# Optimization experiments

Hardware: AMD Instinct MI355X
Metric: run time of the kernel (lower is better)

## Reference

```python
import jax, jax.numpy as jnp
import numpy as np

IMG = 640
C = 256
A = 9
NC = 80
K = 1000          # max candidates kept into NMS (fixed for jit)
SCORE_TH = 0.05
IOU_TH = 0.5
STRIDES = (8, 16, 32, 64, 128)
SIZES = (32, 64, 128, 256, 512)


def conv3(x, w, b):
    # x: [N,C,H,W], w: [O,I,3,3]
    y = jax.lax.conv_general_dilated(x, w, (1, 1), 'SAME',
                                     dimension_numbers=('NCHW', 'OIHW', 'NCHW'))
    return y + b[None, :, None, None]


def head(x, ws, bs, hw, hb):
    for i in range(4):
        x = jax.nn.relu(conv3(x, ws[i], bs[i]))
    return conv3(x, hw, hb)


def classifier(x, ws, bs, hw, hb):
    y = jax.nn.sigmoid(head(x, ws, bs, hw, hb))          # [N, A*NC, H, W]
    n, _, h, w = y.shape
    y = y.transpose(0, 2, 3, 1).reshape(n, h, w, A, NC)  # NHWA,NC ordering as in torch view
    return y.reshape(n, -1, NC)


def regressor(x, ws, bs, hw, hb):
    y = head(x, ws, bs, hw, hb)                           # [N, A*4, H, W]
    n, _, h, w = y.shape
    return y.transpose(0, 2, 3, 1).reshape(n, -1, 4)


def make_anchors():
    ratios = jnp.array([0.5, 1.0, 2.0], jnp.float32)
    scales = jnp.array([1.0, 2.0 ** (1.0 / 3.0), 2.0 ** (2.0 / 3.0)], jnp.float32)
    levels = []
    for stride, size in zip(STRIDES, SIZES):
        ws = (size * scales[None, :]) / jnp.sqrt(ratios[:, None])  # [3,3]
        hs = (size * scales[None, :]) * jnp.sqrt(ratios[:, None])
        ws, hs = ws.reshape(-1), hs.reshape(-1)                    # [9]
        fs = IMG // stride
        c = (jnp.arange(fs, dtype=jnp.float32) + 0.5) * stride
        cy, cx = jnp.meshgrid(c, c, indexing='ij')                 # [H,W]
        cx, cy = cx[..., None], cy[..., None]                      # [H,W,1]
        boxes = jnp.stack([cx - ws / 2, cy - hs / 2, cx + ws / 2, cy + hs / 2], -1)  # [H,W,9,4]
        levels.append(boxes.reshape(-1, 4))
    return jnp.concatenate(levels, 0)  # [76725, 4]


def decode_clip(anchors, loc):
    # BBoxTransform with std (0.1,0.1,0.2,0.2), then ClipBoxes to image
    w = anchors[:, 2] - anchors[:, 0]
    h = anchors[:, 3] - anchors[:, 1]
    cx = anchors[:, 0] + 0.5 * w
    cy = anchors[:, 1] + 0.5 * h
    dx, dy = loc[:, 0] * 0.1, loc[:, 1] * 0.1
    dw, dh = loc[:, 2] * 0.2, loc[:, 3] * 0.2
    pcx, pcy = cx + dx * w, cy + dy * h
    pw, ph = jnp.exp(dw) * w, jnp.exp(dh) * h
    boxes = jnp.stack([pcx - 0.5 * pw, pcy - 0.5 * ph, pcx + 0.5 * pw, pcy + 0.5 * ph], -1)
    return jnp.clip(boxes, 0.0, float(IMG))


def nms_keep(boxes, valid):
    # boxes [K,4] sorted by descending score, valid [K] bool; greedy NMS keep mask
    x1, y1, x2, y2 = boxes[:, 0], boxes[:, 1], boxes[:, 2], boxes[:, 3]
    area = jnp.maximum(x2 - x1, 0.0) * jnp.maximum(y2 - y1, 0.0)
    xx1 = jnp.maximum(x1[:, None], x1[None, :])
    yy1 = jnp.maximum(y1[:, None], y1[None, :])
    xx2 = jnp.minimum(x2[:, None], x2[None, :])
    yy2 = jnp.minimum(y2[:, None], y2[None, :])
    inter = jnp.maximum(xx2 - xx1, 0.0) * jnp.maximum(yy2 - yy1, 0.0)
    iou = inter / (area[:, None] + area[None, :] - inter + 1e-8)
    idx = jnp.arange(boxes.shape[0])

    def body(i, keep):
        sup = (iou[i] > IOU_TH) & (idx > i) & keep[i]
        return keep & ~sup

    return jax.lax.fori_loop(0, boxes.shape[0], body, valid)


def forward(p3, p4, p5, p6, p7, cls_w, cls_b, cls_hw, cls_hb, reg_w, reg_b, reg_hw, reg_hb):
    feats = [p3, p4, p5, p6, p7]
    cls_pred = jnp.concatenate([classifier(f, cls_w, cls_b, cls_hw, cls_hb) for f in feats], 1)[0]  # [N_anch, NC]
    loc_pred = jnp.concatenate([regressor(f, reg_w, reg_b, reg_hw, reg_hb) for f in feats], 1)[0]   # [N_anch, 4]
    anchors = make_anchors()
    boxes = decode_clip(anchors, loc_pred)
    scores = jnp.max(cls_pred, axis=1)                     # [N_anch]
    masked = jnp.where(scores > SCORE_TH, scores, -1.0)
    top_vals, top_idx = jax.lax.top_k(masked, K)
    valid = top_vals > 0.0
    sel_boxes = boxes[top_idx]                             # [K,4]
    keep = nms_keep(sel_boxes, valid)
    sel_cls = cls_pred[top_idx]                            # [K,NC]
    nms_scores = jnp.where(keep, top_vals, 0.0)
    nms_classes = jnp.argmax(sel_cls, axis=1).astype(jnp.int32)
    nms_boxes = jnp.where(keep[:, None], sel_boxes, 0.0)
    return nms_scores, nms_classes, nms_boxes, keep


def setup_inputs() -> dict:
    key = jax.random.key(0)
    ks = jax.random.split(key, 12)
    inp = {}
    for i, (name, hw_) in enumerate(zip(['p3', 'p4', 'p5', 'p6', 'p7'], [80, 40, 20, 10, 5])):
        inp[name] = jax.random.normal(ks[i], (1, C, hw_, hw_), jnp.float32)
    inp['cls_w'] = jax.random.normal(ks[5], (4, C, C, 3, 3), jnp.float32) * 0.05
    inp['cls_b'] = jnp.zeros((4, C), jnp.float32)
    inp['cls_hw'] = jax.random.normal(ks[6], (A * NC, C, 3, 3), jnp.float32) * 0.05
    inp['cls_hb'] = jnp.full((A * NC,), -2.0, jnp.float32)
    inp['reg_w'] = jax.random.normal(ks[7], (4, C, C, 3, 3), jnp.float32) * 0.05
    inp['reg_b'] = jnp.zeros((4, C), jnp.float32)
    inp['reg_hw'] = jax.random.normal(ks[8], (36, C, 3, 3), jnp.float32) * 0.05
    inp['reg_hb'] = jnp.zeros((36,), jnp.float32)
    return inp


def reference(p3, p4, p5, p6, p7, cls_w, cls_b, cls_hw, cls_hb, reg_w, reg_b, reg_hw, reg_hb):
    return forward(p3, p4, p5, p6, p7, cls_w, cls_b, cls_hw, cls_hb, reg_w, reg_b, reg_hw, reg_hb)
```

## Files before the change

### kernel.cpp

```cpp
#include <hip/hip_runtime.h>
#include <math.h>
#include <stdint.h>

#define NANCH 76725
#define NPAD  131072
#define NPAD2 32768
#define PXTOT 8525

typedef _Float16 half8 __attribute__((ext_vector_type(8)));
typedef _Float16 half4 __attribute__((ext_vector_type(4)));
typedef float float4v __attribute__((ext_vector_type(4)));
typedef unsigned long long u64;

#define ACT2_EL  ((size_t)PXTOT * 512)
#define HEADC_EL (720 * PXTOT)
#define HEADR_EL (36 * PXTOT)

#define TRUNK_WP_EL (9 * 2 * 8 * 16 * 64 * 8)
#define CLSH_WP_EL  (9 * 2 * 8 * 48 * 64 * 8)
#define REGH_WP_EL  (9 * 2 * 8 * 4 * 64 * 8)

struct PrepArgs {
    const float* src[10];
    _Float16*    dst[10];
    int Co[10], NC16[10];
    long base[11];
};

__global__ __launch_bounds__(256) void prep_k(PrepArgs P)
{
    long idx = (long)blockIdx.x * 256 + threadIdx.x;
    if (idx >= P.base[10]) return;
    int e = 0;
    while (idx >= P.base[e + 1]) e++;
    long local = idx - P.base[e];
    const int NC16 = P.NC16[e], Co = P.Co[e];
    int lane = (int)(local & 63);
    long t2 = local >> 6;
    int c16 = (int)(t2 % NC16);
    long t3 = t2 / NC16;
    int cc = (int)(t3 & 7);
    int t4 = (int)(t3 >> 3);
    int s = t4 & 1, tap = t4 >> 1;
    int co = c16 * 16 + (lane & 15);
    int kb = cc * 32 + (lane >> 4) * 8;
    const float* src = P.src[e];
    half8 out;
#pragma unroll
    for (int j = 0; j < 8; j++) {
        float v = (co < Co) ? src[(size_t)(co * 256 + kb + j) * 9 + tap] : 0.f;
        _Float16 h = (_Float16)v;
        out[j] = s ? (_Float16)(v - (float)h) : h;
    }
    _Float16* dst = P.dst[e] + ((((size_t)(tap * 2 + s) * 8 + cc) * NC16 + c16) * 64 + lane) * 8;
    *(half8*)dst = out;
}

struct RepArgs { const float* src[5]; _Float16* dst; };

__global__ __launch_bounds__(256) void repack_k(RepArgs R)
{
    __shared__ float T[64][257];
    const int cumT[5] = {100, 125, 132, 134, 135};
    const int Wt[5]   = {80, 40, 20, 10, 5};
    const int pxB[5]  = {0, 6400, 8000, 8400, 8500};
    int t = blockIdx.x;
    int lv = 0; while (t >= cumT[lv]) lv++;
    int tile = t - (lv ? cumT[lv - 1] : 0);
    const int HW = Wt[lv] * Wt[lv];
    const int pxStart = tile * 64;
    const float* src = R.src[lv];
    const int tid = threadIdx.x, w = tid >> 6, l6 = tid & 63;
    int p = pxStart + l6;
    bool ok = p < HW;
    for (int ci = w; ci < 256; ci += 4)
        T[l6][ci] = ok ? src[(size_t)ci * HW + p] : 0.f;
    __syncthreads();
    _Float16* dst = R.dst + (size_t)pxB[lv] * 512;
    for (int px = w; px < 64; px += 4) {
        int pp = pxStart + px;
        if (pp >= HW) continue;
        half4 h, l;
#pragma unroll
        for (int j = 0; j < 4; j++) {
            float v = T[px][l6 * 4 + j];
            _Float16 hh = (_Float16)v;
            h[j] = hh; l[j] = (_Float16)(v - (float)hh);
        }
        *(half4*)(dst + (size_t)pp * 512 + l6 * 4) = h;
        *(half4*)(dst + (size_t)pp * 512 + 256 + l6 * 4) = l;
    }
}

struct C3Args {
    const _Float16* aIn0; const _Float16* aIn1;
    _Float16* aOut0; _Float16* aOut1;
    float* hOut0; float* hOut1;
    const _Float16* wp0; const _Float16* wp1;
    const float* bias0; const float* bias1;
    int CoPad0, CoPad1, Co0, Co1, mode;
};

__global__ __launch_bounds__(256, 4) void conv3_k(C3Args A)
{
    const int cumT[5] = {200, 250, 265, 271, 273};
    const int txA[5]  = {10, 5, 3, 2, 1};
    const int Wt[5]   = {80, 40, 20, 10, 5};
    const int pxB[5]  = {0, 6400, 8000, 8400, 8500};

    __shared__ __align__(16) _Float16 Xs[60 * 72];

    const int gid = blockIdx.x;
    int head, coGrp, t;
    if (A.mode == 0) {
        int oct = gid & 7; head = oct >> 2; int tq = oct & 3;
        int p = gid >> 3; coGrp = p & 1; int tl = p >> 1;
        t = tq * 69 + tl;
    } else {
        int oct = gid & 7; int tq = oct & 3; int ch = oct >> 2;
        int p = gid >> 3; int ci = p & 3; int tl = p >> 2;
        int combo = ch * 4 + ci;
        if (combo >= 7) return;
        head = (combo == 6) ? 1 : 0;
        coGrp = (combo == 6) ? 0 : combo;
        t = tq * 69 + tl;
    }
    if (t >= 273) return;

    int lv = 0; while (t >= cumT[lv]) lv++;
    const int tile = t - (lv ? cumT[lv - 1] : 0);
    const int W = Wt[lv], HW = W * W;
    const int tx = txA[lv];
    const int tyi = tile / tx, txi = tile - tyi * tx;
    const int x0 = txi * 8, y0 = tyi * 4;

    const _Float16* aIn = (head ? A.aIn1 : A.aIn0) + (size_t)pxB[lv] * 512;
    const _Float16* wp  = head ? A.wp1 : A.wp0;
    const float* bias   = head ? A.bias1 : A.bias0;
    const int CoPad     = head ? A.CoPad1 : A.CoPad0;
    const int Co        = head ? A.Co1 : A.Co0;
    const int NC16      = CoPad >> 4;

    const int tid = threadIdx.x;
    const int w = tid >> 6, lane = tid & 63;
    const int l15 = lane & 15, quad = lane >> 4;
    const int coW = coGrp * 128 + w * 32;
    const bool active = coW < CoPad;
    const int c16b = coW >> 4;

    float4v acc[2][2];
#pragma unroll
    for (int i = 0; i < 2; i++)
#pragma unroll
        for (int j = 0; j < 2; j++) acc[i][j] = (float4v){0.f, 0.f, 0.f, 0.f};

    const half8 z8 = {(_Float16)0, (_Float16)0, (_Float16)0, (_Float16)0,
                      (_Float16)0, (_Float16)0, (_Float16)0, (_Float16)0};

    for (int cc = 0; cc < 8; cc++) {
        const int ci0 = cc * 32;
        __syncthreads();
        {
            int u0 = tid, u1 = tid + 256;
            int px0 = u0 >> 3, sg0 = u0 & 7;
            int r0 = px0 / 10, c0 = px0 - r0 * 10;
            int gy0 = y0 + r0 - 1, gx0 = x0 + c0 - 1;
            bool v0ok = (gy0 >= 0) && (gy0 < W) && (gx0 >= 0) && (gx0 < W);
            int e0 = (sg0 < 4) ? (ci0 + sg0 * 8) : (256 + ci0 + (sg0 - 4) * 8);
            int gp0 = v0ok ? (gy0 * W + gx0) : 0;
            half8 v0 = v0ok ? *(const half8*)(aIn + (size_t)gp0 * 512 + e0) : z8;

            bool u1v = u1 < 480;
            int px1 = u1 >> 3, sg1 = u1 & 7;
            int r1 = px1 / 10, c1 = px1 - r1 * 10;
            int gy1 = y0 + r1 - 1, gx1 = x0 + c1 - 1;
            bool v1ok = u1v && (gy1 >= 0) && (gy1 < W) && (gx1 >= 0) && (gx1 < W);
            int e1 = (sg1 < 4) ? (ci0 + sg1 * 8) : (256 + ci0 + (sg1 - 4) * 8);
            int gp1 = v1ok ? (gy1 * W + gx1) : 0;
            half8 v1 = v1ok ? *(const half8*)(aIn + (size_t)gp1 * 512 + e1) : z8;

            *(half8*)(Xs + px0 * 72 + sg0 * 8) = v0;
            if (u1v) *(half8*)(Xs + px1 * 72 + sg1 * 8) = v1;
        }
        __syncthreads();

        if (active) {
            for (int tap = 0; tap < 9; tap++) {
                const int dy = tap / 3 - 1, dx = tap % 3 - 1;
                half8 ah[2], al[2];
#pragma unroll
                for (int mf = 0; mf < 2; mf++) {
                    int lpx = (2 * mf + (l15 >> 3) + 1 + dy) * 10 + (l15 & 7) + 1 + dx;
                    const _Float16* lp = Xs + lpx * 72 + quad * 8;
                    ah[mf] = *(const half8*)lp;
                    al[mf] = *(const half8*)(lp + 32);
                }
                half8 bh[2], bl[2];
#pragma unroll
                for (int nf = 0; nf < 2; nf++) {
                    const _Float16* wb = wp +
                        ((((size_t)(tap * 2) * 8 + cc) * NC16 + c16b + nf) * 64 + lane) * 8;
                    bh[nf] = *(const half8*)wb;
                    bl[nf] = *(const half8*)(wb + (size_t)4096 * NC16);
                }
#pragma unroll
                for (int nf = 0; nf < 2; nf++) {
#pragma unroll
                    for (int mf = 0; mf < 2; mf++) {
                        acc[mf][nf] = __builtin_amdgcn_mfma_f32_16x16x32_f16(ah[mf], bh[nf], acc[mf][nf], 0, 0, 0);
                        acc[mf][nf] = __builtin_amdgcn_mfma_f32_16x16x32_f16(ah[mf], bl[nf], acc[mf][nf], 0, 0, 0);
                        acc[mf][nf] = __builtin_amdgcn_mfma_f32_16x16x32_f16(al[mf], bh[nf], acc[mf][nf], 0, 0, 0);
                    }
                }
            }
        }
    }

    if (!active) return;

    int coN[2];
    float bv[2];
#pragma unroll
    for (int nf = 0; nf < 2; nf++) {
        coN[nf] = coW + nf * 16 + l15;
        bv[nf] = (coN[nf] < Co) ? bias[coN[nf]] : 0.f;
    }

    if (A.mode == 0) {
        _Float16* ao = (head ? A.aOut1 : A.aOut0) + (size_t)pxB[lv] * 512;
#pragma unroll
        for (int nf = 0; nf < 2; nf++) {
#pragma unroll
            for (int mf = 0; mf < 2; mf++) {
#pragma unroll
                for (int r = 0; r < 4; r++) {
                    int m = quad * 4 + r;
                    int yy = y0 + 2 * mf + (m >> 3);
                    int xx = x0 + (m & 7);
                    if (yy < W && xx < W) {
                        int px = yy * W + xx;
                        float v = fmaxf(acc[mf][nf][r] + bv[nf], 0.f);
                        _Float16 h = (_Float16)v;
                        _Float16 lo = (_Float16)(v - (float)h);
                        ao[(size_t)px * 512 + coN[nf]] = h;
                        ao[(size_t)px * 512 + 256 + coN[nf]] = lo;
                    }
                }
            }
        }
    } else {
        float* ho = (head ? A.hOut1 : A.hOut0) + (size_t)Co * pxB[lv];
#pragma unroll
        for (int nf = 0; nf < 2; nf++) {
            if (coN[nf] < Co) {
                float* col = ho + (size_t)coN[nf] * HW;
#pragma unroll
                for (int mf = 0; mf < 2; mf++) {
#pragma unroll
                    for (int r = 0; r < 4; r++) {
                        int m = quad * 4 + r;
                        int yy = y0 + 2 * mf + (m >> 3);
                        int xx = x0 + (m & 7);
                        if (yy < W && xx < W) col[yy * W + xx] = acc[mf][nf][r] + bv[nf];
                    }
                }
            }
        }
    }
}

__global__ void cls_reduce_k(const float* __restrict__ ho,
                             u64* __restrict__ keys, int* __restrict__ cls_all)
{
    const int cumB[5] = {225, 282, 297, 301, 302};
    const int HWs[5]  = {6400, 1600, 400, 100, 25};
    const int pxB[5]  = {0, 6400, 8000, 8400, 8500};
    const int offs[5] = {0, 57600, 72000, 75600, 76500};
    int b = blockIdx.x;
    int lv = 0;
    while (b >= cumB[lv]) lv++;
    int local = (b - (lv ? cumB[lv - 1] : 0)) * 256 + threadIdx.x;
    const int HW = HWs[lv];
    if (local >= HW * 9) return;
    int a = local / HW, p = local - a * HW;
    const float* base = ho + (size_t)720 * pxB[lv] + (size_t)a * 80 * HW + p;
    float m = -1.f; int arg = 0;
    for (int c = 0; c < 80; c++) {
        float logit = base[(size_t)c * HW];
        float s = 1.0f / (1.0f + expf(-logit));
        if (s > m) { m = s; arg = c; }
    }
    float masked = (m > 0.05f) ? m : -1.0f;
    unsigned u = __float_as_uint(masked);
    unsigned su = (u & 0x80000000u) ? ~u : (u | 0x80000000u);
    int g = offs[lv] + p * 9 + a;
    keys[g] = ((u64)su << 32) | (u64)(0xFFFFFFFFu - (unsigned)g);
    cls_all[g] = arg;
}

struct DecArgs { float aw[45]; float ah[45]; };

__global__ void decode_k(const float* __restrict__ ro, DecArgs D, float* __restrict__ boxes_all)
{
    const int cumB[5] = {225, 282, 297, 301, 302};
    const int HWs[5]  = {6400, 1600, 400, 100, 25};
    const int Wt[5]   = {80, 40, 20, 10, 5};
    const int pxB[5]  = {0, 6400, 8000, 8400, 8500};
    const int offs[5] = {0, 57600, 72000, 75600, 76500};
    const float strd[5] = {8.f, 16.f, 32.f, 64.f, 128.f};
    int b = blockIdx.x;
    int lv = 0;
    while (b >= cumB[lv]) lv++;
    int local = (b - (lv ? cumB[lv - 1] : 0)) * 256 + threadIdx.x;
    const int HW = HWs[lv], W = Wt[lv];
    if (local >= HW * 9) return;
    int a = local / HW, p = local - a * HW;
    int y = p / W, x = p - y * W;
    float cx0 = ((float)x + 0.5f) * strd[lv];
    float cy0 = ((float)y + 0.5f) * strd[lv];
    float aw = D.aw[lv * 9 + a], ahh = D.ah[lv * 9 + a];
    float ax1 = cx0 - aw * 0.5f, ax2 = cx0 + aw * 0.5f;
    float ay1 = cy0 - ahh * 0.5f, ay2 = cy0 + ahh * 0.5f;
    float w = ax2 - ax1, h = ay2 - ay1;
    float cx = ax1 + 0.5f * w, cy = ay1 + 0.5f * h;
    const float* base = ro + (size_t)36 * pxB[lv] + p;
    float l0 = base[(size_t)(a * 4 + 0) * HW];
    float l1 = base[(size_t)(a * 4 + 1) * HW];
    float l2 = base[(size_t)(a * 4 + 2) * HW];
    float l3 = base[(size_t)(a * 4 + 3) * HW];
    float dx = l0 * 0.1f, dy = l1 * 0.1f, dw = l2 * 0.2f, dh = l3 * 0.2f;
    float pcx = cx + dx * w, pcy = cy + dy * h;
    float pw = expf(dw) * w, ph = expf(dh) * h;
    float bx1 = fminf(fmaxf(pcx - 0.5f * pw, 0.f), 640.f);
    float by1 = fminf(fmaxf(pcy - 0.5f * ph, 0.f), 640.f);
    float bx2 = fminf(fmaxf(pcx + 0.5f * pw, 0.f), 640.f);
    float by2 = fminf(fmaxf(pcy + 0.5f * ph, 0.f), 640.f);
    int g = offs[lv] + p * 9 + a;
    boxes_all[g * 4 + 0] = bx1;
    boxes_all[g * 4 + 1] = by1;
    boxes_all[g * 4 + 2] = bx2;
    boxes_all[g * 4 + 3] = by2;
}

__global__ void pad_keys_k(u64* __restrict__ keys)
{
    int i = blockIdx.x * blockDim.x + threadIdx.x + NANCH;
    if (i < NPAD) keys[i] = 0ULL;
}

__global__ __launch_bounds__(1024) void chunk_sort_desc_k(u64* __restrict__ keys)
{
    __shared__ u64 s[4096];
    const int base = blockIdx.x * 4096;
    for (int i = threadIdx.x; i < 4096; i += 1024) s[i] = keys[base + i];
    __syncthreads();
    for (int size = 2; size <= 4096; size <<= 1) {
        for (int stride = size >> 1; stride > 0; stride >>= 1) {
            for (int t = threadIdx.x; t < 2048; t += 1024) {
                int low = t & (stride - 1);
                int i = ((t - low) << 1) | low;
                int j = i + stride;
                bool desc = ((i & size) == 0);
                u64 a = s[i], b = s[j];
                if (desc ? (a < b) : (a > b)) { s[i] = b; s[j] = a; }
            }
            __syncthreads();
        }
    }
    for (int i = threadIdx.x; i < 4096; i += 1024) keys[base + i] = s[i];
}

__global__ __launch_bounds__(1024) void gather_top_k(const u64* __restrict__ keys,
                                                     u64* __restrict__ keys2)
{
    int i = blockIdx.x * 1024 + threadIdx.x;
    keys2[i] = keys[(i >> 10) * 4096 + (i & 1023)];
}

__global__ void bitonic_global_k(u64* __restrict__ keys, int size, int stride)
{
    int t = blockIdx.x * blockDim.x + threadIdx.x;
    int low = t & (stride - 1);
    int i = ((t - low) << 1) | low;
    int j = i + stride;
    bool desc = ((i & size) == 0);
    u64 a = keys[i], b = keys[j];
    if (desc ? (a < b) : (a > b)) { keys[i] = b; keys[j] = a; }
}

__global__ __launch_bounds__(1024) void bitonic_local_full_k(u64* __restrict__ keys)
{
    __shared__ u64 s[4096];
    const int base = blockIdx.x * 4096;
    for (int i = threadIdx.x; i < 4096; i += 1024) s[i] = keys[base + i];
    __syncthreads();
    for (int size = 2; size <= 4096; size <<= 1) {
        for (int stride = size >> 1; stride > 0; stride >>= 1) {
            for (int t = threadIdx.x; t < 2048; t += 1024) {
                int low = t & (stride - 1);
                int i = ((t - low) << 1) | low;
                int j = i + stride;
                bool desc = (((base + i) & size) == 0);
                u64 a = s[i], b = s[j];
                if (desc ? (a < b) : (a > b)) { s[i] = b; s[j] = a; }
            }
            __syncthreads();
        }
    }
    for (int i = threadIdx.x; i < 4096; i += 1024) keys[base + i] = s[i];
}

__global__ __launch_bounds__(1024) void bitonic_local_k(u64* __restrict__ keys, int size)
{
    __shared__ u64 s[4096];
    const int base = blockIdx.x * 4096;
    for (int i = threadIdx.x; i < 4096; i += 1024) s[i] = keys[base + i];
    __syncthreads();
    const bool desc = ((base & size) == 0);
    for (int stride = 2048; stride > 0; stride >>= 1) {
        for (int t = threadIdx.x; t < 2048; t += 1024) {
            int low = t & (stride - 1);
            int i = ((t - low) << 1) | low;
            int j = i + stride;
            u64 a = s[i], b = s[j];
            if (desc ? (a < b) : (a > b)) { s[i] = b; s[j] = a; }
        }
        __syncthreads();
    }
    for (int i = threadIdx.x; i < 4096; i += 1024) keys[base + i] = s[i];
}

__global__ void gather_cand_k(const u64* __restrict__ keys,
                              const float* __restrict__ boxes_all,
                              const int* __restrict__ cls_all,
                              float* __restrict__ cand)
{
    int i = blockIdx.x * 256 + threadIdx.x;
    if (i >= 1000) return;
    u64 k = keys[i];
    unsigned shi = (unsigned)(k >> 32);
    unsigned u = (shi & 0x80000000u) ? (shi ^ 0x80000000u) : ~shi;
    float val = __uint_as_float(u);
    int anchor = (int)(0xFFFFFFFFu - (unsigned)(k & 0xFFFFFFFFull));
    float x1 = boxes_all[anchor * 4 + 0];
    float y1 = boxes_all[anchor * 4 + 1];
    float x2 = boxes_all[anchor * 4 + 2];
    float y2 = boxes_all[anchor * 4 + 3];
    cand[i * 8 + 0] = x1;
    cand[i * 8 + 1] = y1;
    cand[i * 8 + 2] = x2;
    cand[i * 8 + 3] = y2;
    cand[i * 8 + 4] = fmaxf(x2 - x1, 0.f) * fmaxf(y2 - y1, 0.f);
    cand[i * 8 + 5] = val;
    cand[i * 8 + 6] = (float)cls_all[anchor];
    cand[i * 8 + 7] = (val > 0.0f) ? 1.f : 0.f;
}

__global__ __launch_bounds__(256) void iou_mask_k(const float* __restrict__ cand,
                                                  u64* __restrict__ mask)
{
    const int i = blockIdx.x;
    const float x1 = cand[i * 8 + 0], y1 = cand[i * 8 + 1];
    const float x2 = cand[i * 8 + 2], y2 = cand[i * 8 + 3];
    const float ar = cand[i * 8 + 4];
    const int tid = threadIdx.x;
    const int wave = tid >> 6, lane = tid & 63;
    for (int base = 0; base < 1024; base += 256) {
        int j = base + tid;
        bool sup = false;
        if (j < 1000 && j > i) {
            float jx1 = cand[j * 8 + 0], jy1 = cand[j * 8 + 1];
            float jx2 = cand[j * 8 + 2], jy2 = cand[j * 8 + 3];
            float jar = cand[j * 8 + 4];
            float xx1 = fmaxf(x1, jx1), yy1 = fmaxf(y1, jy1);
            float xx2 = fminf(x2, jx2), yy2 = fminf(y2, jy2);
            float inter = fmaxf(xx2 - xx1, 0.f) * fmaxf(yy2 - yy1, 0.f);
            float iou = inter / (ar + jar - inter + 1e-8f);
            sup = iou > 0.5f;
        }
        u64 ball = __ballot(sup);
        int word = (base >> 6) + wave;
        if (lane == 0) mask[(size_t)i * 16 + word] = ball;
    }
}

__global__ __launch_bounds__(64) void nms_sweep_out_k(const float* __restrict__ cand,
                                                      const u64* __restrict__ M,
                                                      float* __restrict__ out)
{
    const int lane = threadIdx.x;

    u64 V[16];
#pragma unroll
    for (int t = 0; t < 16; t++) {
        int i = t * 64 + lane;
        bool v = (i < 1000) && (cand[i * 8 + 7] > 0.f);
        V[t] = __ballot(v);
    }

    u64 pend[16];
#pragma unroll
    for (int t = 0; t < 16; t++) pend[t] = 0;
    u64 aliveW[16];

    for (int T = 0; T < 16; T++) {
        u64 rw[16];
        int row = T * 64 + lane;
        for (int t = T; t < 16; t++)
            rw[t] = (row < 1000) ? M[(size_t)row * 16 + t] : 0ULL;

        u64 s = pend[T];
        u64 alive = 0;
        u64 myw = rw[T];
        const u64 VT = V[T];
#pragma unroll
        for (int i = 0; i < 64; i++) {
            u64 ri = __shfl(myw, i);
            bool a = ((VT >> i) & 1) && !((s >> i) & 1);
            if (a) { s |= ri; alive |= (1ULL << i); }
        }
        aliveW[T] = alive;

        for (int t = T + 1; t < 16; t++) {
            u64 c = ((alive >> lane) & 1) ? rw[t] : 0ULL;
#pragma unroll
            for (int d = 1; d < 64; d <<= 1) c |= __shfl_xor(c, d);
            pend[t] |= c;
        }
    }

    for (int i = lane; i < 1000; i += 64) {
        int kp = (int)((aliveW[i >> 6] >> (i & 63)) & 1);
        float m = kp ? 1.f : 0.f;
        out[i] = kp ? cand[i * 8 + 5] : 0.f;
        out[1000 + i] = cand[i * 8 + 6];
        out[2000 + i * 4 + 0] = m * cand[i * 8 + 0];
        out[2000 + i * 4 + 1] = m * cand[i * 8 + 1];
        out[2000 + i * 4 + 2] = m * cand[i * 8 + 2];
        out[2000 + i * 4 + 3] = m * cand[i * 8 + 3];
        out[6000 + i] = m;
    }
}

extern "C" void kernel_launch(void* const* d_in, const int* in_sizes, int n_in,
                              void* d_out, int out_size, void* d_ws, size_t ws_size,
                              hipStream_t stream)
{
    const float* feats[5];
    for (int i = 0; i < 5; i++) feats[i] = (const float*)d_in[i];
    const float* cls_w  = (const float*)d_in[5];
    const float* cls_b  = (const float*)d_in[6];
    const float* cls_hw = (const float*)d_in[7];
    const float* cls_hb = (const float*)d_in[8];
    const float* reg_w  = (const float*)d_in[9];
    const float* reg_b  = (const float*)d_in[10];
    const float* reg_hw = (const float*)d_in[11];
    const float* reg_hb = (const float*)d_in[12];
    float* out = (float*)d_out;

    char* ws = (char*)d_ws;
    size_t off = 0;
    auto alloc = [&](size_t sz) { size_t o = off; off += (sz + 255) & ~(size_t)255; return o; };

    size_t R0 = alloc((size_t)(HEADC_EL + HEADR_EL) * 4);
    _Float16* act2_feats = (_Float16*)(ws + R0);
    float* headout_cls = (float*)(ws + R0);
    float* headout_reg = headout_cls + HEADC_EL;

    _Float16* a2_clsA = (_Float16*)(ws + alloc(ACT2_EL * 2));
    _Float16* a2_regA = (_Float16*)(ws + alloc(ACT2_EL * 2));
    _Float16* a2_clsB = (_Float16*)(ws + alloc(ACT2_EL * 2));
    _Float16* a2_regB = (_Float16*)(ws + alloc(ACT2_EL * 2));

    _Float16* wpc[4]; _Float16* wpr[4];
    for (int i = 0; i < 4; i++) wpc[i] = (_Float16*)(ws + alloc((size_t)TRUNK_WP_EL * 2));
    _Float16* wpch = (_Float16*)(ws + alloc((size_t)CLSH_WP_EL * 2));
    for (int i = 0; i < 4; i++) wpr[i] = (_Float16*)(ws + alloc((size_t)TRUNK_WP_EL * 2));
    _Float16* wprh = (_Float16*)(ws + alloc((size_t)REGH_WP_EL * 2));

    u64* keys  = (u64*)(ws + alloc((size_t)NPAD * 8));
    u64* keys2 = (u64*)(ws + alloc((size_t)NPAD2 * 8));
    float* boxes_all = (float*)(ws + alloc((size_t)NANCH * 16));
    int* cls_all = (int*)(ws + alloc((size_t)NANCH * 4));
    float* cand = (float*)(ws + alloc((size_t)1000 * 8 * 4));
    u64* mask = (u64*)(ws + alloc((size_t)1000 * 16 * 8));
    (void)ws_size;

    PrepArgs P;
    long cum = 0;
    for (int e = 0; e < 10; e++) {
        const float* src; _Float16* dst; int Co, NC16;
        if (e < 4)      { src = cls_w + (size_t)e * 589824; dst = wpc[e]; Co = 256; NC16 = 16; }
        else if (e == 4){ src = cls_hw;                     dst = wpch;   Co = 720; NC16 = 48; }
        else if (e < 9) { src = reg_w + (size_t)(e - 5) * 589824; dst = wpr[e - 5]; Co = 256; NC16 = 16; }
        else            { src = reg_hw;                     dst = wprh;   Co = 36;  NC16 = 4; }
        P.src[e] = src; P.dst[e] = dst; P.Co[e] = Co; P.NC16[e] = NC16;
        P.base[e] = cum; cum += (long)9216 * NC16;
    }
    P.base[10] = cum;
    prep_k<<<(int)((cum + 255) / 256), 256, 0, stream>>>(P);

    pad_keys_k<<<(NPAD - NANCH + 255) / 256, 256, 0, stream>>>(keys);

    RepArgs R;
    for (int lv = 0; lv < 5; lv++) R.src[lv] = feats[lv];
    R.dst = act2_feats;
    repack_k<<<135, 256, 0, stream>>>(R);

    auto trunk = [&](const _Float16* i0, const _Float16* i1, _Float16* o0, _Float16* o1,
                     const _Float16* w0, const _Float16* w1, const float* b0, const float* b1) {
        C3Args C;
        C.aIn0 = i0; C.aIn1 = i1; C.aOut0 = o0; C.aOut1 = o1;
        C.hOut0 = nullptr; C.hOut1 = nullptr;
        C.wp0 = w0; C.wp1 = w1; C.bias0 = b0; C.bias1 = b1;
        C.CoPad0 = 256; C.CoPad1 = 256;
        C.Co0 = 256; C.Co1 = 256; C.mode = 0;
        conv3_k<<<8 * 2 * 69, 256, 0, stream>>>(C);
    };
    trunk(act2_feats, act2_feats, a2_clsA, a2_regA, wpc[0], wpr[0], cls_b + 0,   reg_b + 0);
    trunk(a2_clsA,    a2_regA,    a2_clsB, a2_regB, wpc[1], wpr[1], cls_b + 256, reg_b + 256);
    trunk(a2_clsB,    a2_regB,    a2_clsA, a2_regA, wpc[2], wpr[2], cls_b + 512, reg_b + 512);
    trunk(a2_clsA,    a2_regA,    a2_clsB, a2_regB, wpc[3], wpr[3], cls_b + 768, reg_b + 768);

    {
        C3Args C;
        C.aIn0 = a2_clsB; C.aIn1 = a2_regB;
        C.aOut0 = nullptr; C.aOut1 = nullptr;
        C.hOut0 = headout_cls; C.hOut1 = headout_reg;
        C.wp0 = wpch; C.wp1 = wprh; C.bias0 = cls_hb; C.bias1 = reg_hb;
        C.CoPad0 = 768; C.CoPad1 = 64;
        C.Co0 = 720; C.Co1 = 36; C.mode = 1;
        conv3_k<<<8 * 4 * 69, 256, 0, stream>>>(C);
    }

    cls_reduce_k<<<302, 256, 0, stream>>>(headout_cls, keys, cls_all);

    DecArgs D;
    {
        const float sz[5] = {32.f, 64.f, 128.f, 256.f, 512.f};
        const float ratios[3] = {0.5f, 1.0f, 2.0f};
        const float scales[3] = {1.0f, 1.25992104989487316477f, 1.58740105196819947475f};
        for (int lv = 0; lv < 5; lv++)
            for (int r = 0; r < 3; r++)
                for (int s = 0; s < 3; s++) {
                    D.aw[lv * 9 + r * 3 + s] = sz[lv] * scales[s] / sqrtf(ratios[r]);
                    D.ah[lv * 9 + r * 3 + s] = sz[lv] * scales[s] * sqrtf(ratios[r]);
                }
    }
    decode_k<<<302, 256, 0, stream>>>(headout_reg, D, boxes_all);

    chunk_sort_desc_k<<<NPAD / 4096, 1024, 0, stream>>>(keys);
    gather_top_k<<<NPAD2 / 1024, 1024, 0, stream>>>(keys, keys2);
    bitonic_local_full_k<<<NPAD2 / 4096, 1024, 0, stream>>>(keys2);
    for (int size = 8192; size <= NPAD2; size <<= 1) {
        for (int stride = size >> 1; stride >= 4096; stride >>= 1)
            bitonic_global_k<<<NPAD2 / 2 / 1024, 1024, 0, stream>>>(keys2, size, stride);
        bitonic_local_k<<<NPAD2 / 4096, 1024, 0, stream>>>(keys2, size);
    }

    gather_cand_k<<<4, 256, 0, stream>>>(keys2, boxes_all, cls_all, cand);
    iou_mask_k<<<1000, 256, 0, stream>>>(cand, mask);
    nms_sweep_out_k<<<1, 64, 0, stream>>>(cand, mask, out);
}
```

Measured before the change: 864.2 us.

## Prefetch activation tiles and weight fragments, swizzle LDS layout in conv kernel

Moves the global loads of the next input-channel chunk into registers right after the barrier, so they overlap the MFMA work of the current chunk. Weight fragments for the next tap are also loaded one step ahead (double-buffered in registers). The LDS tile layout is swizzled by XORing the 8-element slot with the pixel index to cut bank conflicts on fragment reads. The cost is more registers held live, which may lower occupancy.

```diff
diff --git a/kernel.cpp b/kernel.cpp
--- a/kernel.cpp
+++ b/kernel.cpp
@@ -157,32 +157,50 @@
     const half8 z8 = {(_Float16)0, (_Float16)0, (_Float16)0, (_Float16)0,
                       (_Float16)0, (_Float16)0, (_Float16)0, (_Float16)0};
 
+    const int u0 = tid, u1 = tid + 256;
+    const int px0 = u0 >> 3, sg0 = u0 & 7;
+    const int rA = px0 / 10, cA = px0 - rA * 10;
+    const int gy0 = y0 + rA - 1, gx0 = x0 + cA - 1;
+    const bool v0ok = (gy0 >= 0) && (gy0 < W) && (gx0 >= 0) && (gx0 < W);
+    const _Float16* ga0 = aIn + (size_t)(v0ok ? (gy0 * W + gx0) : 0) * 512
+                          + ((sg0 < 4) ? sg0 * 8 : 256 + (sg0 - 4) * 8);
+    _Float16* ls0 = Xs + px0 * 72 + ((sg0 & 4) ? 32 : 0) + ((((sg0 & 3) + px0) & 3) * 8);
+
+    const bool u1v = u1 < 480;
+    const int px1 = u1 >> 3, sg1 = u1 & 7;
+    const int rB = px1 / 10, cB = px1 - rB * 10;
+    const int gy1 = y0 + rB - 1, gx1 = x0 + cB - 1;
+    const bool v1ok = u1v && (gy1 >= 0) && (gy1 < W) && (gx1 >= 0) && (gx1 < W);
+    const _Float16* ga1 = aIn + (size_t)(v1ok ? (gy1 * W + gx1) : 0) * 512
+                          + ((sg1 < 4) ? sg1 * 8 : 256 + (sg1 - 4) * 8);
+    _Float16* ls1 = Xs + px1 * 72 + ((sg1 & 4) ? 32 : 0) + ((((sg1 & 3) + px1) & 3) * 8);
+
+    half8 st0 = v0ok ? *(const half8*)ga0 : z8;
+    half8 st1 = v1ok ? *(const half8*)ga1 : z8;
+
+    const size_t wsplit = (size_t)4096 * NC16;
+    auto loadB = [&](int cc, int tap, half8* bh, half8* bl) {
+#pragma unroll
+        for (int nf = 0; nf < 2; nf++) {
+            const _Float16* wb = wp +
+                ((((size_t)(tap * 2) * 8 + cc) * NC16 + c16b + nf) * 64 + lane) * 8;
+            bh[nf] = *(const half8*)wb;
+            bl[nf] = *(const half8*)(wb + wsplit);
+        }
+    };
+
+    half8 bhc[2], blc[2], bhn[2], bln[2];
+    if (active) loadB(0, 0, bhc, blc);
+
     for (int cc = 0; cc < 8; cc++) {
-        const int ci0 = cc * 32;
         __syncthreads();
-        {
-            int u0 = tid, u1 = tid + 256;
-            int px0 = u0 >> 3, sg0 = u0 & 7;
-            int r0 = px0 / 10, c0 = px0 - r0 * 10;
-            int gy0 = y0 + r0 - 1, gx0 = x0 + c0 - 1;
-            bool v0ok = (gy0 >= 0) && (gy0 < W) && (gx0 >= 0) && (gx0 < W);
-            int e0 = (sg0 < 4) ? (ci0 + sg0 * 8) : (256 + ci0 + (sg0 - 4) * 8);
-            int gp0 = v0ok ? (gy0 * W + gx0) : 0;
-            half8 v0 = v0ok ? *(const half8*)(aIn + (size_t)gp0 * 512 + e0) : z8;
-
-            bool u1v = u1 < 480;
-            int px1 = u1 >> 3, sg1 = u1 & 7;
-            int r1 = px1 / 10, c1 = px1 - r1 * 10;
-            int gy1 = y0 + r1 - 1, gx1 = x0 + c1 - 1;
-            bool v1ok = u1v && (gy1 >= 0) && (gy1 < W) && (gx1 >= 0) && (gx1 < W);
-            int e1 = (sg1 < 4) ? (ci0 + sg1 * 8) : (256 + ci0 + (sg1 - 4) * 8);
-            int gp1 = v1ok ? (gy1 * W + gx1) : 0;
-            half8 v1 = v1ok ? *(const half8*)(aIn + (size_t)gp1 * 512 + e1) : z8;
-
-            *(half8*)(Xs + px0 * 72 + sg0 * 8) = v0;
-            if (u1v) *(half8*)(Xs + px1 * 72 + sg1 * 8) = v1;
-        }
+        *(half8*)ls0 = st0;
+        if (u1v) *(half8*)ls1 = st1;
         __syncthreads();
+        if (cc < 7) {
+            st0 = v0ok ? *(const half8*)(ga0 + (cc + 1) * 32) : z8;
+            st1 = v1ok ? *(const half8*)(ga1 + (cc + 1) * 32) : z8;
+        }
 
         if (active) {
             for (int tap = 0; tap < 9; tap++) {
@@ -191,27 +209,23 @@
 #pragma unroll
                 for (int mf = 0; mf < 2; mf++) {
                     int lpx = (2 * mf + (l15 >> 3) + 1 + dy) * 10 + (l15 & 7) + 1 + dx;
-                    const _Float16* lp = Xs + lpx * 72 + quad * 8;
+                    const _Float16* lp = Xs + lpx * 72 + (((quad + lpx) & 3) * 8);
                     ah[mf] = *(const half8*)lp;
                     al[mf] = *(const half8*)(lp + 32);
                 }
-                half8 bh[2], bl[2];
+                if (tap < 8) loadB(cc, tap + 1, bhn, bln);
+                else if (cc < 7) loadB(cc + 1, 0, bhn, bln);
 #pragma unroll
                 for (int nf = 0; nf < 2; nf++) {
-                    const _Float16* wb = wp +
-                        ((((size_t)(tap * 2) * 8 + cc) * NC16 + c16b + nf) * 64 + lane) * 8;
-                    bh[nf] = *(const half8*)wb;
-                    bl[nf] = *(const half8*)(wb + (size_t)4096 * NC16);
-                }
-#pragma unroll
-                for (int nf = 0; nf < 2; nf++) {
 #pragma unroll
                     for (int mf = 0; mf < 2; mf++) {
-                        acc[mf][nf] = __builtin_amdgcn_mfma_f32_16x16x32_f16(ah[mf], bh[nf], acc[mf][nf], 0, 0, 0);
-                        acc[mf][nf] = __builtin_amdgcn_mfma_f32_16x16x32_f16(ah[mf], bl[nf], acc[mf][nf], 0, 0, 0);
-                        acc[mf][nf] = __builtin_amdgcn_mfma_f32_16x16x32_f16(al[mf], bh[nf], acc[mf][nf], 0, 0, 0);
+                        acc[mf][nf] = __builtin_amdgcn_mfma_f32_16x16x32_f16(ah[mf], bhc[nf], acc[mf][nf], 0, 0, 0);
+                        acc[mf][nf] = __builtin_amdgcn_mfma_f32_16x16x32_f16(ah[mf], blc[nf], acc[mf][nf], 0, 0, 0);
+                        acc[mf][nf] = __builtin_amdgcn_mfma_f32_16x16x32_f16(al[mf], bhc[nf], acc[mf][nf], 0, 0, 0);
                     }
                 }
+#pragma unroll
+                for (int nf = 0; nf < 2; nf++) { bhc[nf] = bhn[nf]; blc[nf] = bln[nf]; }
             }
         }
     }
```

Result: slower. 1.065 ms (+23.2%).
